# Kernel tuning notes

Hardware: AMD Instinct MI355X
Metric: run time of the kernel (lower is better)

The kernel has to match this reference:

```python
import jax, jax.numpy as jnp
import numpy as np

NUM_LEVELS = 16
LEVEL_DIM = 2
BASE_RES = 16
DESIRED_RES = 2048
HASHMAP_SIZE = 2 ** 19
MULTIRES = 6
N_POINTS = 1048576

_scale = np.exp2(np.log2(DESIRED_RES / BASE_RES) / (NUM_LEVELS - 1))
RESOLUTIONS = [int(np.ceil(BASE_RES * _scale ** l)) for l in range(NUM_LEVELS)]
PRIMES = np.array([1, 2654435761, 805459861], dtype=np.uint32)
CORNERS = np.array([[i, j, k] for i in (0, 1) for j in (0, 1) for k in (0, 1)], dtype=np.int32)  # [8,3]


def positional_embed(x):
    # NeRF embedding (include_input, log-sampled freqs 2^0..2^(M-1)) -> [N, 3 + 3*2*M] = [N,39]
    freqs = (2.0 ** jnp.arange(MULTIRES)).astype(x.dtype)        # [M]
    xb = x[:, None, :] * freqs[None, :, None]                    # [N, M, 3]
    emb = jnp.concatenate([jnp.sin(xb), jnp.cos(xb)], axis=-1)   # [N, M, 6]
    return jnp.concatenate([x, emb.reshape(x.shape[0], -1)], axis=-1)


def hash_encode(x, tables):
    # multiresolution hash-grid trilinear lookup; x in [0,1]^3 -> [N, NUM_LEVELS*LEVEL_DIM]
    corners = jnp.asarray(CORNERS)       # [8,3]
    primes = jnp.asarray(PRIMES)         # [3] uint32
    outs = []
    for l, R in enumerate(RESOLUTIONS):  # fixed 16 levels (structurally distinct)
        pos = x * (R - 1)                # [N,3]
        p0 = jnp.floor(pos)
        w = pos - p0                     # fractional part, [N,3]
        c = p0.astype(jnp.int32)[:, None, :] + corners[None]   # [N,8,3] corner coords
        c = jnp.clip(c, 0, R - 1)
        if (R ** 3) <= HASHMAP_SIZE:
            idx = c[..., 0] + R * c[..., 1] + R * R * c[..., 2]  # direct (dense) indexing
        else:
            cu = c.astype(jnp.uint32)
            h = (cu[..., 0] * primes[0]) ^ (cu[..., 1] * primes[1]) ^ (cu[..., 2] * primes[2])
            idx = (h & jnp.uint32(HASHMAP_SIZE - 1)).astype(jnp.int32)
        wc = jnp.where(corners[None].astype(bool), w[:, None, :], 1.0 - w[:, None, :])  # [N,8,3]
        wc = jnp.prod(wc, axis=-1)        # trilinear weights [N,8]
        feats = tables[l][idx]            # gather [N,8,LEVEL_DIM]
        outs.append(jnp.sum(wc[..., None] * feats, axis=1))
    return jnp.concatenate(outs, axis=-1)


def softplus100(x):
    # torch.nn.Softplus(beta=100) with default threshold=20 (linear when beta*x > 20)
    return jnp.where(x * 100.0 > 20.0, x, jax.nn.softplus(x * 100.0) / 100.0)


def setup_inputs() -> dict:
    key = jax.random.key(0)
    ks = jax.random.split(key, 8)
    D_IN = 3 + 3 * 2 * MULTIRES + NUM_LEVELS * LEVEL_DIM  # 71
    x = jax.random.uniform(ks[0], (N_POINTS, 3), dtype=jnp.float32)
    tables = jax.random.uniform(ks[1], (NUM_LEVELS, HASHMAP_SIZE, LEVEL_DIM), minval=-1e-4, maxval=1e-4, dtype=jnp.float32)
    W0 = jax.random.normal(ks[2], (64, D_IN), dtype=jnp.float32) * (np.sqrt(2.0) / np.sqrt(64.0))
    b0 = jnp.zeros((64,), jnp.float32)
    W1 = jax.random.normal(ks[3], (64, 64), dtype=jnp.float32) * (np.sqrt(2.0) / np.sqrt(64.0))
    b1 = jnp.zeros((64,), jnp.float32)
    W2 = jnp.full((17, 64), np.sqrt(np.pi) / np.sqrt(64.0), jnp.float32) + jax.random.normal(ks[4], (17, 64), dtype=jnp.float32) * 1e-4
    b2 = jnp.full((17,), -1.0, jnp.float32)  # geometric init bias
    return {"x": x, "tables": tables, "W0": W0, "b0": b0, "W1": W1, "b1": b1, "W2": W2, "b2": b2}


def reference(x, tables, W0, b0, W1, b1, W2, b2):
    # divide_factor = 1.0 -> encoding sees x directly
    feat = hash_encode(x, tables)                                   # [N,32]
    h = jnp.concatenate([positional_embed(x), feat], axis=-1)       # [N,71]
    h = softplus100(h @ W0.T + b0)                                  # [N,64]
    h = softplus100(h @ W1.T + b1)                                  # [N,64]
    return h @ W2.T + b2                                            # [N,17] = (sdf, 16 features)
```

## Files before the change

kernel.cpp:

```cpp
#include <hip/hip_runtime.h>
#include <stdint.h>

#define HMAP   (1u << 19)
#define HMASK  (HMAP - 1u)

typedef short bf16x8 __attribute__((ext_vector_type(8)));
typedef float f32x4  __attribute__((ext_vector_type(4)));
typedef float f32x2  __attribute__((ext_vector_type(2)));
typedef unsigned u32x2 __attribute__((ext_vector_type(2)));

__device__ __constant__ const int c_res[16] = {16, 23, 31, 43, 59, 81, 112, 154, 213, 295, 407, 562, 777, 1073, 1483, 2048};

__device__ __forceinline__ unsigned short f2bf(float f) {
    unsigned u = __float_as_uint(f);
    u += 0x7fffu + ((u >> 16) & 1u);
    return (unsigned short)(u >> 16);
}

__device__ __forceinline__ float softplus100(float v) {
    return fmaxf(v, 0.f) + 0.01f * __logf(1.f + __expf(-100.f * fabsf(v)));
}

__device__ __forceinline__ bf16x8 cvt8(const float* __restrict__ p) {
    f32x4 a = *(const f32x4*)p;
    f32x4 b = *(const f32x4*)(p + 4);
    bf16x8 r;
    r[0] = f2bf(a[0]); r[1] = f2bf(a[1]); r[2] = f2bf(a[2]); r[3] = f2bf(a[3]);
    r[4] = f2bf(b[0]); r[5] = f2bf(b[1]); r[6] = f2bf(b[2]); r[7] = f2bf(b[3]);
    return r;
}

__device__ __forceinline__ float2 upk(unsigned v) {
    return make_float2(__uint_as_float(v << 16), __uint_as_float(v & 0xffff0000u));
}

__device__ __forceinline__ float2 gather_level(const float* __restrict__ tab, int R,
                                               float x0, float x1, float x2) {
    const float Rm1 = (float)(R - 1);
    float px = x0 * Rm1, py = x1 * Rm1, pz = x2 * Rm1;
    float fx = floorf(px), fy = floorf(py), fz = floorf(pz);
    float wx = px - fx, wy = py - fy, wz = pz - fz;
    int ix = (int)fx, iy = (int)fy, iz = (int)fz;
    ix = max(0, min(ix, R - 1)); iy = max(0, min(iy, R - 1)); iz = max(0, min(iz, R - 1));
    int jx = min(ix + 1, R - 1), jy = min(iy + 1, R - 1), jz = min(iz + 1, R - 1);
    float ax = 1.f - wx, ay = 1.f - wy, az = 1.f - wz;
    float wyz0 = ay * az, wyz1 = wy * az, wyz2 = ay * wz, wyz3 = wy * wz;
    float2 lo[4], hi[4];
    const bool adj = (jx == ix + 1);
    if ((long long)R * R * R <= (long long)HMAP) {
        unsigned sy = (unsigned)R, sz = (unsigned)(R * R);
        unsigned bases[4] = {(unsigned)iy * sy + (unsigned)iz * sz,
                             (unsigned)jy * sy + (unsigned)iz * sz,
                             (unsigned)iy * sy + (unsigned)jz * sz,
                             (unsigned)jy * sy + (unsigned)jz * sz};
        const float2* t2 = (const float2*)tab;
        #pragma unroll
        for (int k = 0; k < 4; ++k) {
            unsigned i0 = bases[k] + (unsigned)ix;
            if (adj && !(i0 & 1u)) {
                f32x4 q = *(const f32x4*)(tab + ((size_t)i0 << 1));
                lo[k] = make_float2(q[0], q[1]);
                hi[k] = make_float2(q[2], q[3]);
            } else {
                lo[k] = t2[i0];
                hi[k] = t2[bases[k] + (unsigned)jx];
            }
        }
    } else {
        unsigned hy0 = (unsigned)iy * 2654435761u, hy1 = (unsigned)jy * 2654435761u;
        unsigned hz0 = (unsigned)iz * 805459861u,  hz1 = (unsigned)jz * 805459861u;
        unsigned ms[4] = {hy0 ^ hz0, hy1 ^ hz0, hy0 ^ hz1, hy1 ^ hz1};
        if (adj && ((ix & 1) == 0)) {
            #pragma unroll
            for (int k = 0; k < 4; ++k) {
                unsigned h = ((unsigned)ix ^ ms[k]) & HMASK;
                f32x4 q = *(const f32x4*)(tab + ((size_t)(h & ~1u) << 1));
                float2 e0 = make_float2(q[0], q[1]);
                float2 e1 = make_float2(q[2], q[3]);
                bool sw = (h & 1u) != 0;
                lo[k] = sw ? e1 : e0;
                hi[k] = sw ? e0 : e1;
            }
        } else {
            const float2* t2 = (const float2*)tab;
            #pragma unroll
            for (int k = 0; k < 4; ++k) {
                unsigned hl = ((unsigned)ix ^ ms[k]) & HMASK;
                unsigned hh = ((unsigned)jx ^ ms[k]) & HMASK;
                lo[k] = t2[hl];
                hi[k] = t2[hh];
            }
        }
    }
    float2 r = make_float2(0.f, 0.f);
    float wyz[4] = {wyz0, wyz1, wyz2, wyz3};
    #pragma unroll
    for (int k = 0; k < 4; ++k) {
        float wl = ax * wyz[k], wh = wx * wyz[k];
        r.x += wl * lo[k].x + wh * hi[k].x;
        r.y += wl * lo[k].y + wh * hi[k].y;
    }
    return r;
}

__device__ __forceinline__ void gather2(const float* __restrict__ tab, int R,
                                        float x0A, float x1A, float x2A,
                                        float x0B, float x1B, float x2B,
                                        float2& rA, float2& rB) {
    const float Rm1 = (float)(R - 1);
    float wxv[2], axv[2];
    float wyz[2][4];
    float2 lo[2][4], hi[2][4];
    int ixv[2], jxv[2];
    unsigned basev[2][4];
    const bool dense = (long long)R * R * R <= (long long)HMAP;
    #pragma unroll
    for (int t = 0; t < 2; ++t) {
        const float X0 = t ? x0B : x0A, X1 = t ? x1B : x1A, X2 = t ? x2B : x2A;
        float px = X0 * Rm1, py = X1 * Rm1, pz = X2 * Rm1;
        float fx = floorf(px), fy = floorf(py), fz = floorf(pz);
        float wx = px - fx, wy = py - fy, wz = pz - fz;
        int ix = (int)fx, iy = (int)fy, iz = (int)fz;
        ix = max(0, min(ix, R - 1)); iy = max(0, min(iy, R - 1)); iz = max(0, min(iz, R - 1));
        int jx = min(ix + 1, R - 1), jy = min(iy + 1, R - 1), jz = min(iz + 1, R - 1);
        float ax = 1.f - wx, ay = 1.f - wy, az = 1.f - wz;
        wyz[t][0] = ay * az; wyz[t][1] = wy * az; wyz[t][2] = ay * wz; wyz[t][3] = wy * wz;
        wxv[t] = wx; axv[t] = ax; ixv[t] = ix; jxv[t] = jx;
        if (dense) {
            unsigned sy = (unsigned)R, sz = (unsigned)(R * R);
            basev[t][0] = (unsigned)iy * sy + (unsigned)iz * sz;
            basev[t][1] = (unsigned)jy * sy + (unsigned)iz * sz;
            basev[t][2] = (unsigned)iy * sy + (unsigned)jz * sz;
            basev[t][3] = (unsigned)jy * sy + (unsigned)jz * sz;
        } else {
            unsigned hy0 = (unsigned)iy * 2654435761u, hy1 = (unsigned)jy * 2654435761u;
            unsigned hz0 = (unsigned)iz * 805459861u,  hz1 = (unsigned)jz * 805459861u;
            basev[t][0] = hy0 ^ hz0; basev[t][1] = hy1 ^ hz0;
            basev[t][2] = hy0 ^ hz1; basev[t][3] = hy1 ^ hz1;
        }
    }
    if (dense) {
        const float2* t2 = (const float2*)tab;
        #pragma unroll
        for (int t = 0; t < 2; ++t) {
            const bool adj = (jxv[t] == ixv[t] + 1);
            #pragma unroll
            for (int k = 0; k < 4; ++k) {
                unsigned i0 = basev[t][k] + (unsigned)ixv[t];
                if (adj && !(i0 & 1u)) {
                    f32x4 q = *(const f32x4*)(tab + ((size_t)i0 << 1));
                    lo[t][k] = make_float2(q[0], q[1]);
                    hi[t][k] = make_float2(q[2], q[3]);
                } else {
                    lo[t][k] = t2[i0];
                    hi[t][k] = t2[basev[t][k] + (unsigned)jxv[t]];
                }
            }
        }
    } else {
        const float2* t2 = (const float2*)tab;
        #pragma unroll
        for (int t = 0; t < 2; ++t) {
            const bool adj = (jxv[t] == ixv[t] + 1) && ((ixv[t] & 1) == 0);
            #pragma unroll
            for (int k = 0; k < 4; ++k) {
                if (adj) {
                    unsigned h = ((unsigned)ixv[t] ^ basev[t][k]) & HMASK;
                    f32x4 q = *(const f32x4*)(tab + ((size_t)(h & ~1u) << 1));
                    float2 e0 = make_float2(q[0], q[1]);
                    float2 e1 = make_float2(q[2], q[3]);
                    bool sw = (h & 1u) != 0;
                    lo[t][k] = sw ? e1 : e0;
                    hi[t][k] = sw ? e0 : e1;
                } else {
                    unsigned hl = ((unsigned)ixv[t] ^ basev[t][k]) & HMASK;
                    unsigned hh = ((unsigned)jxv[t] ^ basev[t][k]) & HMASK;
                    lo[t][k] = t2[hl];
                    hi[t][k] = t2[hh];
                }
            }
        }
    }
    float2 res[2];
    #pragma unroll
    for (int t = 0; t < 2; ++t) {
        float2 r = make_float2(0.f, 0.f);
        #pragma unroll
        for (int k = 0; k < 4; ++k) {
            float wl = axv[t] * wyz[t][k], wh = wxv[t] * wyz[t][k];
            r.x += wl * lo[t][k].x + wh * hi[t][k].x;
            r.y += wl * lo[t][k].y + wh * hi[t][k].y;
        }
        res[t] = r;
    }
    rA = res[0]; rB = res[1];
}

__device__ __forceinline__ void gather2h(const unsigned* __restrict__ tab, int R,
                                         float x0A, float x1A, float x2A,
                                         float x0B, float x1B, float x2B,
                                         float2& rA, float2& rB) {
    const float Rm1 = (float)(R - 1);
    float wxv[2], axv[2], wyz[2][4];
    int ixv[2], jxv[2];
    bool adjv[2];
    unsigned msv[2][4];
    #pragma unroll
    for (int t = 0; t < 2; ++t) {
        const float X0 = t ? x0B : x0A, X1 = t ? x1B : x1A, X2 = t ? x2B : x2A;
        float px = X0 * Rm1, py = X1 * Rm1, pz = X2 * Rm1;
        float fx = floorf(px), fy = floorf(py), fz = floorf(pz);
        float wx = px - fx, wy = py - fy, wz = pz - fz;
        int ix = (int)fx, iy = (int)fy, iz = (int)fz;
        ix = max(0, min(ix, R - 1)); iy = max(0, min(iy, R - 1)); iz = max(0, min(iz, R - 1));
        int jx = min(ix + 1, R - 1), jy = min(iy + 1, R - 1), jz = min(iz + 1, R - 1);
        float ax = 1.f - wx, ay = 1.f - wy, az = 1.f - wz;
        wyz[t][0] = ay * az; wyz[t][1] = wy * az; wyz[t][2] = ay * wz; wyz[t][3] = wy * wz;
        wxv[t] = wx; axv[t] = ax; ixv[t] = ix; jxv[t] = jx;
        adjv[t] = (jx == ix + 1) && ((ix & 1) == 0);
        unsigned hy0 = (unsigned)iy * 2654435761u, hy1 = (unsigned)jy * 2654435761u;
        unsigned hz0 = (unsigned)iz * 805459861u,  hz1 = (unsigned)jz * 805459861u;
        msv[t][0] = hy0 ^ hz0; msv[t][1] = hy1 ^ hz0;
        msv[t][2] = hy0 ^ hz1; msv[t][3] = hy1 ^ hz1;
    }
    float2 lo[2][4], hi[2][4];
    #pragma unroll
    for (int t = 0; t < 2; ++t) {
        #pragma unroll
        for (int k = 0; k < 4; ++k) {
            if (adjv[t]) {
                unsigned h = ((unsigned)ixv[t] ^ msv[t][k]) & HMASK;
                u32x2 q = *(const u32x2*)(tab + (h & ~1u));
                float2 e0 = upk(q[0]), e1 = upk(q[1]);
                bool sw = (h & 1u) != 0;
                lo[t][k] = sw ? e1 : e0;
                hi[t][k] = sw ? e0 : e1;
            } else {
                unsigned hl = ((unsigned)ixv[t] ^ msv[t][k]) & HMASK;
                unsigned hh = ((unsigned)jxv[t] ^ msv[t][k]) & HMASK;
                lo[t][k] = upk(tab[hl]);
                hi[t][k] = upk(tab[hh]);
            }
        }
    }
    float2 res[2];
    #pragma unroll
    for (int t = 0; t < 2; ++t) {
        float2 r = make_float2(0.f, 0.f);
        #pragma unroll
        for (int k = 0; k < 4; ++k) {
            float wl = axv[t] * wyz[t][k], wh = wxv[t] * wyz[t][k];
            r.x += wl * lo[t][k].x + wh * hi[t][k].x;
            r.y += wl * lo[t][k].y + wh * hi[t][k].y;
        }
        res[t] = r;
    }
    rA = res[0]; rB = res[1];
}

__global__ __launch_bounds__(256)
void cvt_tables(const float* __restrict__ tables, unsigned* __restrict__ tbf) {
    const size_t i = (size_t)blockIdx.x * 256 + threadIdx.x;
    const f32x2* src = (const f32x2*)(tables + (size_t)5 * 2 * HMAP);
    f32x2 f = __builtin_nontemporal_load(src + i);
    unsigned v = (unsigned)f2bf(f[0]) | ((unsigned)f2bf(f[1]) << 16);
    __builtin_nontemporal_store(v, tbf + i);
}

__global__ __launch_bounds__(256, 6)
void gather_hashed(const float* __restrict__ x, const unsigned* __restrict__ tbf,
                   unsigned* __restrict__ feat, int N) {
    const int j = blockIdx.x & 7;
    const int i = blockIdx.x >> 3;
    int level, chunk;
    if (i < 2048) {
        level = 5 + j; chunk = i;
    } else {
        const int r = i - 2048;
        if (j < 3) {
            const int share = (j == 2) ? 682 : 683;
            if (r >= share) return;
            level = 13; chunk = j * 683 + r;
        } else if (j < 6) {
            const int jj = j - 3;
            const int share = (jj == 2) ? 682 : 683;
            if (r >= share) return;
            level = 14; chunk = jj * 683 + r;
        } else {
            if (r >= 1024) return;
            level = 15; chunk = (j - 6) * 1024 + r;
        }
    }
    const size_t p0 = (size_t)chunk * 512 + 2u * threadIdx.x;
    const f32x2* xv = (const f32x2*)(x + 3 * p0);
    f32x2 u0 = __builtin_nontemporal_load(xv);
    f32x2 u1 = __builtin_nontemporal_load(xv + 1);
    f32x2 u2 = __builtin_nontemporal_load(xv + 2);
    float2 fA, fB;
    gather2h(tbf + (size_t)(level - 5) * HMAP, c_res[level],
             u0[0], u0[1], u1[0],
             u1[1], u2[0], u2[1],
             fA, fB);
    u32x2 v;
    v[0] = (unsigned)f2bf(fA.x) | ((unsigned)f2bf(fA.y) << 16);
    v[1] = (unsigned)f2bf(fB.x) | ((unsigned)f2bf(fB.y) << 16);
    __builtin_nontemporal_store(v, (u32x2*)(feat + (size_t)(level - 5) * N + p0));
}

#define NPB       128
#define TILES     8
#define PTS_BLK   (NPB * TILES)
#define SA_STRIDE 104
#define SW0_OFF   (128 * 104)
#define SMEM_SHORTS (SW0_OFF + 64 * 104)

__global__ __launch_bounds__(256, 4)
void mlp_tiled2(const float* __restrict__ x, const float* __restrict__ tables,
                const unsigned* __restrict__ feat,
                const float* __restrict__ W0, const float* __restrict__ b0,
                const float* __restrict__ W1, const float* __restrict__ b1,
                const float* __restrict__ W2, const float* __restrict__ b2,
                float* __restrict__ out, int N) {
    __shared__ unsigned short smem[SMEM_SHORTS];
    const int tid  = threadIdx.x;
    const int blk  = blockIdx.x;
    const int wave = tid >> 6, lane = tid & 63;
    const int mhalf = (wave & 1) * 64;
    const int nhalf = (wave >> 1);
    const int lrow = lane & 15, quad = lane >> 4;

    for (int i = tid; i < 64 * 104; i += 256) {
        int n = i / 104, k = i - n * 104;
        smem[SW0_OFF + i] = (k < 71) ? f2bf(W0[n * 71 + k]) : (unsigned short)0;
    }
    for (int i = tid; i < 128 * 25; i += 256) {
        int p = i / 25, k = i - p * 25;
        smem[p * SA_STRIDE + 71 + k] = 0;
    }
    bf16x8 w1f[2][2];
    #pragma unroll
    for (int ks = 0; ks < 2; ++ks)
        #pragma unroll
        for (int nt = 0; nt < 2; ++nt) {
            int n = nhalf * 32 + nt * 16 + lrow;
            w1f[ks][nt] = cvt8(W1 + n * 64 + ks * 32 + quad * 8);
        }
    bf16x8 w2f[2];
    {
        int n2 = nhalf * 16 + lrow;
        #pragma unroll
        for (int ks = 0; ks < 2; ++ks) {
            if (n2 < 17) w2f[ks] = cvt8(W2 + n2 * 64 + ks * 32 + quad * 8);
            else { bf16x8 z = {0,0,0,0,0,0,0,0}; w2f[ks] = z; }
        }
    }
    float b0v[2], b1v[2], b2v;
    #pragma unroll
    for (int nt = 0; nt < 2; ++nt) {
        b0v[nt] = b0[nhalf * 32 + nt * 16 + lrow];
        b1v[nt] = b1[nhalf * 32 + nt * 16 + lrow];
    }
    { int c2 = nhalf * 16 + lrow; b2v = (c2 < 17) ? b2[c2] : 0.f; }
    __syncthreads();

    const size_t pbase0 = (size_t)blk * PTS_BLK;
    #pragma unroll 1
    for (int t = 0; t < TILES; ++t) {
        const size_t pb = pbase0 + (size_t)t * NPB;
        {
            const int p = tid & 127;
            const size_t gp = pb + p;
            unsigned short* row = &smem[p * SA_STRIDE];
            const float x0 = __builtin_nontemporal_load(x + 3 * gp);
            const float x1 = __builtin_nontemporal_load(x + 3 * gp + 1);
            const float x2 = __builtin_nontemporal_load(x + 3 * gp + 2);
            float sa, ca, sb, cb, sc, cc;
            __sincosf(x0, &sa, &ca);
            __sincosf(x1, &sb, &cb);
            __sincosf(x2, &sc, &cc);
            if (tid < 128) {
                row[0] = f2bf(x0); row[1] = f2bf(x1); row[2] = f2bf(x2);
                #pragma unroll
                for (int m = 0; m < 6; ++m) {
                    row[3 + 6 * m + 0] = f2bf(sa);
                    row[3 + 6 * m + 1] = f2bf(sb);
                    row[3 + 6 * m + 2] = f2bf(sc);
                    float nsa = 2.f * sa * ca, nca = 1.f - 2.f * sa * sa;
                    float nsb = 2.f * sb * cb, ncb = 1.f - 2.f * sb * sb;
                    float nsc = 2.f * sc * cc, ncc = 1.f - 2.f * sc * sc;
                    sa = nsa; ca = nca; sb = nsb; cb = ncb; sc = nsc; cc = ncc;
                }
                float2 f;
                f = gather_level(tables,                         16, x0, x1, x2);
                row[39] = f2bf(f.x); row[40] = f2bf(f.y);
                f = gather_level(tables + (size_t)1 * 2 * HMAP,  23, x0, x1, x2);
                row[41] = f2bf(f.x); row[42] = f2bf(f.y);
                f = gather_level(tables + (size_t)2 * 2 * HMAP,  31, x0, x1, x2);
                row[43] = f2bf(f.x); row[44] = f2bf(f.y);
            } else {
                #pragma unroll
                for (int m = 0; m < 6; ++m) {
                    row[3 + 6 * m + 3] = f2bf(ca);
                    row[3 + 6 * m + 4] = f2bf(cb);
                    row[3 + 6 * m + 5] = f2bf(cc);
                    float nsa = 2.f * sa * ca, nca = 1.f - 2.f * sa * sa;
                    float nsb = 2.f * sb * cb, ncb = 1.f - 2.f * sb * sb;
                    float nsc = 2.f * sc * cc, ncc = 1.f - 2.f * sc * sc;
                    sa = nsa; ca = nca; sb = nsb; cb = ncb; sc = nsc; cc = ncc;
                }
                float2 f;
                f = gather_level(tables + (size_t)3 * 2 * HMAP,  43, x0, x1, x2);
                row[45] = f2bf(f.x); row[46] = f2bf(f.y);
                f = gather_level(tables + (size_t)4 * 2 * HMAP,  59, x0, x1, x2);
                row[47] = f2bf(f.x); row[48] = f2bf(f.y);
                #pragma unroll
                for (int li = 0; li < 11; ++li) {
                    unsigned v = __builtin_nontemporal_load(feat + (size_t)li * N + gp);
                    row[49 + 2 * li] = (unsigned short)(v & 0xffffu);
                    row[50 + 2 * li] = (unsigned short)(v >> 16);
                }
            }
        }
        __syncthreads();

        f32x4 acc0[4][2];
        #pragma unroll
        for (int mt = 0; mt < 4; ++mt)
            #pragma unroll
            for (int nt = 0; nt < 2; ++nt) acc0[mt][nt] = (f32x4){0.f, 0.f, 0.f, 0.f};
        #pragma unroll
        for (int ks = 0; ks < 3; ++ks) {
            bf16x8 bfr[2];
            #pragma unroll
            for (int nt = 0; nt < 2; ++nt) {
                int n = nhalf * 32 + nt * 16 + lrow;
                bfr[nt] = *(const bf16x8*)&smem[SW0_OFF + n * 104 + ks * 32 + quad * 8];
            }
            #pragma unroll
            for (int mt = 0; mt < 4; ++mt) {
                int m = mhalf + mt * 16 + lrow;
                bf16x8 afr = *(const bf16x8*)&smem[m * SA_STRIDE + ks * 32 + quad * 8];
                #pragma unroll
                for (int nt = 0; nt < 2; ++nt)
                    acc0[mt][nt] = __builtin_amdgcn_mfma_f32_16x16x32_bf16(afr, bfr[nt], acc0[mt][nt], 0, 0, 0);
            }
        }
        __syncthreads();
        #pragma unroll
        for (int mt = 0; mt < 4; ++mt)
            #pragma unroll
            for (int nt = 0; nt < 2; ++nt) {
                int colg = nhalf * 32 + nt * 16 + lrow;
                #pragma unroll
                for (int r = 0; r < 4; ++r) {
                    int rowm = mhalf + mt * 16 + quad * 4 + r;
                    smem[rowm * SA_STRIDE + colg] = f2bf(softplus100(acc0[mt][nt][r] + b0v[nt]));
                }
            }
        __syncthreads();

        f32x4 acc1[4][2];
        #pragma unroll
        for (int mt = 0; mt < 4; ++mt)
            #pragma unroll
            for (int nt = 0; nt < 2; ++nt) acc1[mt][nt] = (f32x4){0.f, 0.f, 0.f, 0.f};
        #pragma unroll
        for (int ks = 0; ks < 2; ++ks) {
            #pragma unroll
            for (int mt = 0; mt < 4; ++mt) {
                int m = mhalf + mt * 16 + lrow;
                bf16x8 afr = *(const bf16x8*)&smem[m * SA_STRIDE + ks * 32 + quad * 8];
                #pragma unroll
                for (int nt = 0; nt < 2; ++nt)
                    acc1[mt][nt] = __builtin_amdgcn_mfma_f32_16x16x32_bf16(afr, w1f[ks][nt], acc1[mt][nt], 0, 0, 0);
            }
        }
        __syncthreads();
        #pragma unroll
        for (int mt = 0; mt < 4; ++mt)
            #pragma unroll
            for (int nt = 0; nt < 2; ++nt) {
                int colg = nhalf * 32 + nt * 16 + lrow;
                #pragma unroll
                for (int r = 0; r < 4; ++r) {
                    int rowm = mhalf + mt * 16 + quad * 4 + r;
                    smem[rowm * SA_STRIDE + colg] = f2bf(softplus100(acc1[mt][nt][r] + b1v[nt]));
                }
            }
        __syncthreads();

        f32x4 acc2[4];
        #pragma unroll
        for (int mt = 0; mt < 4; ++mt) acc2[mt] = (f32x4){0.f, 0.f, 0.f, 0.f};
        #pragma unroll
        for (int ks = 0; ks < 2; ++ks) {
            #pragma unroll
            for (int mt = 0; mt < 4; ++mt) {
                int m = mhalf + mt * 16 + lrow;
                bf16x8 afr = *(const bf16x8*)&smem[m * SA_STRIDE + ks * 32 + quad * 8];
                acc2[mt] = __builtin_amdgcn_mfma_f32_16x16x32_bf16(afr, w2f[ks], acc2[mt], 0, 0, 0);
            }
        }
        {
            int colg = nhalf * 16 + lrow;
            if (colg < 17) {
                #pragma unroll
                for (int mt = 0; mt < 4; ++mt)
                    #pragma unroll
                    for (int r = 0; r < 4; ++r) {
                        int rowm = mhalf + mt * 16 + quad * 4 + r;
                        __builtin_nontemporal_store(acc2[mt][r] + b2v,
                                                    out + (pb + rowm) * 17 + colg);
                    }
            }
        }
        __syncthreads();
    }
}

__global__ __launch_bounds__(256, 6)
void gather_levels(const float* __restrict__ x, const float* __restrict__ tables,
                   unsigned* __restrict__ feat, int N, int C) {
    const int b = blockIdx.x;
    const int half = 8 * C;
    int r, level;
    if (b < half) { r = b; level = r & 7; }
    else          { r = b - half; level = 15 - (r & 7); }
    const size_t p0 = (size_t)(r >> 3) * 512 + 2u * threadIdx.x;
    const f32x2* xv = (const f32x2*)(x + 3 * p0);
    f32x2 u0 = __builtin_nontemporal_load(xv);
    f32x2 u1 = __builtin_nontemporal_load(xv + 1);
    f32x2 u2 = __builtin_nontemporal_load(xv + 2);
    float2 fA, fB;
    gather2(tables + (size_t)level * (2u * HMAP), c_res[level],
            u0[0], u0[1], u1[0],
            u1[1], u2[0], u2[1],
            fA, fB);
    u32x2 v;
    v[0] = (unsigned)f2bf(fA.x) | ((unsigned)f2bf(fA.y) << 16);
    v[1] = (unsigned)f2bf(fB.x) | ((unsigned)f2bf(fB.y) << 16);
    __builtin_nontemporal_store(v, (u32x2*)(feat + (size_t)level * N + p0));
}

__global__ __launch_bounds__(256, 4)
void mlp_tiled(const float* __restrict__ x, const unsigned* __restrict__ feat,
               const float* __restrict__ W0, const float* __restrict__ b0,
               const float* __restrict__ W1, const float* __restrict__ b1,
               const float* __restrict__ W2, const float* __restrict__ b2,
               float* __restrict__ out, int N) {
    __shared__ unsigned short smem[SMEM_SHORTS];
    const int tid  = threadIdx.x;
    const int blk  = blockIdx.x;
    const int wave = tid >> 6, lane = tid & 63;
    const int mhalf = (wave & 1) * 64;
    const int nhalf = (wave >> 1);
    const int lrow = lane & 15, quad = lane >> 4;

    for (int i = tid; i < 64 * 104; i += 256) {
        int n = i / 104, k = i - n * 104;
        smem[SW0_OFF + i] = (k < 71) ? f2bf(W0[n * 71 + k]) : (unsigned short)0;
    }
    for (int i = tid; i < 128 * 25; i += 256) {
        int p = i / 25, k = i - p * 25;
        smem[p * SA_STRIDE + 71 + k] = 0;
    }
    bf16x8 w1f[2][2];
    #pragma unroll
    for (int ks = 0; ks < 2; ++ks)
        #pragma unroll
        for (int nt = 0; nt < 2; ++nt) {
            int n = nhalf * 32 + nt * 16 + lrow;
            w1f[ks][nt] = cvt8(W1 + n * 64 + ks * 32 + quad * 8);
        }
    bf16x8 w2f[2];
    {
        int n2 = nhalf * 16 + lrow;
        #pragma unroll
        for (int ks = 0; ks < 2; ++ks) {
            if (n2 < 17) w2f[ks] = cvt8(W2 + n2 * 64 + ks * 32 + quad * 8);
            else { bf16x8 z = {0,0,0,0,0,0,0,0}; w2f[ks] = z; }
        }
    }
    float b0v[2], b1v[2], b2v;
    #pragma unroll
    for (int nt = 0; nt < 2; ++nt) {
        b0v[nt] = b0[nhalf * 32 + nt * 16 + lrow];
        b1v[nt] = b1[nhalf * 32 + nt * 16 + lrow];
    }
    { int c2 = nhalf * 16 + lrow; b2v = (c2 < 17) ? b2[c2] : 0.f; }
    __syncthreads();

    const size_t pbase0 = (size_t)blk * PTS_BLK;
    #pragma unroll 1
    for (int t = 0; t < TILES; ++t) {
        const size_t pb = pbase0 + (size_t)t * NPB;
        {
            const int p = tid & 127;
            const size_t gp = pb + p;
            unsigned short* row = &smem[p * SA_STRIDE];
            const float x0 = __builtin_nontemporal_load(x + 3 * gp);
            const float x1 = __builtin_nontemporal_load(x + 3 * gp + 1);
            const float x2 = __builtin_nontemporal_load(x + 3 * gp + 2);
            if (tid < 128) {
                row[0] = f2bf(x0); row[1] = f2bf(x1); row[2] = f2bf(x2);
                float fr = 1.f;
                #pragma unroll
                for (int m = 0; m < 6; ++m) {
                    row[3 + 6 * m + 0] = f2bf(__sinf(x0 * fr));
                    row[3 + 6 * m + 1] = f2bf(__sinf(x1 * fr));
                    row[3 + 6 * m + 2] = f2bf(__sinf(x2 * fr));
                    fr *= 2.f;
                }
            } else {
                float fr = 1.f;
                #pragma unroll
                for (int m = 0; m < 6; ++m) {
                    row[3 + 6 * m + 3] = f2bf(__cosf(x0 * fr));
                    row[3 + 6 * m + 4] = f2bf(__cosf(x1 * fr));
                    row[3 + 6 * m + 5] = f2bf(__cosf(x2 * fr));
                    fr *= 2.f;
                }
                #pragma unroll
                for (int l = 0; l < 16; ++l) {
                    unsigned v = __builtin_nontemporal_load(feat + (size_t)l * N + gp);
                    row[39 + 2 * l] = (unsigned short)(v & 0xffffu);
                    row[40 + 2 * l] = (unsigned short)(v >> 16);
                }
            }
        }
        __syncthreads();

        f32x4 acc0[4][2];
        #pragma unroll
        for (int mt = 0; mt < 4; ++mt)
            #pragma unroll
            for (int nt = 0; nt < 2; ++nt) acc0[mt][nt] = (f32x4){0.f, 0.f, 0.f, 0.f};
        #pragma unroll
        for (int ks = 0; ks < 3; ++ks) {
            bf16x8 bfr[2];
            #pragma unroll
            for (int nt = 0; nt < 2; ++nt) {
                int n = nhalf * 32 + nt * 16 + lrow;
                bfr[nt] = *(const bf16x8*)&smem[SW0_OFF + n * 104 + ks * 32 + quad * 8];
            }
            #pragma unroll
            for (int mt = 0; mt < 4; ++mt) {
                int m = mhalf + mt * 16 + lrow;
                bf16x8 afr = *(const bf16x8*)&smem[m * SA_STRIDE + ks * 32 + quad * 8];
                #pragma unroll
                for (int nt = 0; nt < 2; ++nt)
                    acc0[mt][nt] = __builtin_amdgcn_mfma_f32_16x16x32_bf16(afr, bfr[nt], acc0[mt][nt], 0, 0, 0);
            }
        }
        __syncthreads();
        #pragma unroll
        for (int mt = 0; mt < 4; ++mt)
            #pragma unroll
            for (int nt = 0; nt < 2; ++nt) {
                int colg = nhalf * 32 + nt * 16 + lrow;
                #pragma unroll
                for (int r = 0; r < 4; ++r) {
                    int rowm = mhalf + mt * 16 + quad * 4 + r;
                    smem[rowm * SA_STRIDE + colg] = f2bf(softplus100(acc0[mt][nt][r] + b0v[nt]));
                }
            }
        __syncthreads();

        f32x4 acc1[4][2];
        #pragma unroll
        for (int mt = 0; mt < 4; ++mt)
            #pragma unroll
            for (int nt = 0; nt < 2; ++nt) acc1[mt][nt] = (f32x4){0.f, 0.f, 0.f, 0.f};
        #pragma unroll
        for (int ks = 0; ks < 2; ++ks) {
            #pragma unroll
            for (int mt = 0; mt < 4; ++mt) {
                int m = mhalf + mt * 16 + lrow;
                bf16x8 afr = *(const bf16x8*)&smem[m * SA_STRIDE + ks * 32 + quad * 8];
                #pragma unroll
                for (int nt = 0; nt < 2; ++nt)
                    acc1[mt][nt] = __builtin_amdgcn_mfma_f32_16x16x32_bf16(afr, w1f[ks][nt], acc1[mt][nt], 0, 0, 0);
            }
        }
        __syncthreads();
        #pragma unroll
        for (int mt = 0; mt < 4; ++mt)
            #pragma unroll
            for (int nt = 0; nt < 2; ++nt) {
                int colg = nhalf * 32 + nt * 16 + lrow;
                #pragma unroll
                for (int r = 0; r < 4; ++r) {
                    int rowm = mhalf + mt * 16 + quad * 4 + r;
                    smem[rowm * SA_STRIDE + colg] = f2bf(softplus100(acc1[mt][nt][r] + b1v[nt]));
                }
            }
        __syncthreads();

        f32x4 acc2[4];
        #pragma unroll
        for (int mt = 0; mt < 4; ++mt) acc2[mt] = (f32x4){0.f, 0.f, 0.f, 0.f};
        #pragma unroll
        for (int ks = 0; ks < 2; ++ks) {
            #pragma unroll
            for (int mt = 0; mt < 4; ++mt) {
                int m = mhalf + mt * 16 + lrow;
                bf16x8 afr = *(const bf16x8*)&smem[m * SA_STRIDE + ks * 32 + quad * 8];
                acc2[mt] = __builtin_amdgcn_mfma_f32_16x16x32_bf16(afr, w2f[ks], acc2[mt], 0, 0, 0);
            }
        }
        {
            int colg = nhalf * 16 + lrow;
            if (colg < 17) {
                #pragma unroll
                for (int mt = 0; mt < 4; ++mt)
                    #pragma unroll
                    for (int r = 0; r < 4; ++r) {
                        int rowm = mhalf + mt * 16 + quad * 4 + r;
                        __builtin_nontemporal_store(acc2[mt][r] + b2v,
                                                    out + (pb + rowm) * 17 + colg);
                    }
            }
        }
        __syncthreads();
    }
}

__global__ __launch_bounds__(256, 3)
void gn_fused(const float* __restrict__ x, const float* __restrict__ tables,
              const float* __restrict__ W0, const float* __restrict__ b0,
              const float* __restrict__ W1, const float* __restrict__ b1,
              const float* __restrict__ W2, const float* __restrict__ b2,
              float* __restrict__ out) {
    __shared__ unsigned short smem[SMEM_SHORTS];
    const int tid = threadIdx.x;
    const int blk = blockIdx.x;
    const int wave = tid >> 6, lane = tid & 63;
    const int mhalf = (wave & 1) * 64;
    const int nhalf = (wave >> 1);
    const int lrow = lane & 15, quad = lane >> 4;
    for (int i = tid; i < 64 * 104; i += 256) {
        int n = i / 104, k = i - n * 104;
        smem[SW0_OFF + i] = (k < 71) ? f2bf(W0[n * 71 + k]) : (unsigned short)0;
    }
    for (int i = tid; i < 128 * 25; i += 256) {
        int p = i / 25, k = i - p * 25;
        smem[p * SA_STRIDE + 71 + k] = 0;
    }
    bf16x8 w1f[2][2];
    #pragma unroll
    for (int ks = 0; ks < 2; ++ks)
        #pragma unroll
        for (int nt = 0; nt < 2; ++nt) {
            int n = nhalf * 32 + nt * 16 + lrow;
            w1f[ks][nt] = cvt8(W1 + n * 64 + ks * 32 + quad * 8);
        }
    bf16x8 w2f[2];
    {
        int n2 = nhalf * 16 + lrow;
        #pragma unroll
        for (int ks = 0; ks < 2; ++ks) {
            if (n2 < 17) w2f[ks] = cvt8(W2 + n2 * 64 + ks * 32 + quad * 8);
            else { bf16x8 z = {0,0,0,0,0,0,0,0}; w2f[ks] = z; }
        }
    }
    float b0v[2], b1v[2], b2v;
    #pragma unroll
    for (int nt = 0; nt < 2; ++nt) {
        b0v[nt] = b0[nhalf * 32 + nt * 16 + lrow];
        b1v[nt] = b1[nhalf * 32 + nt * 16 + lrow];
    }
    { int c2 = nhalf * 16 + lrow; b2v = (c2 < 17) ? b2[c2] : 0.f; }
    {
        const int p = tid & 127;
        const size_t gp = (size_t)blk * NPB + p;
        const float x0 = x[3 * gp], x1 = x[3 * gp + 1], x2 = x[3 * gp + 2];
        unsigned short* row = &smem[p * SA_STRIDE];
        if (tid < 128) {
            row[0] = f2bf(x0); row[1] = f2bf(x1); row[2] = f2bf(x2);
            float fr = 1.f;
            #pragma unroll
            for (int m = 0; m < 6; ++m) {
                row[3 + 6 * m + 0] = f2bf(__sinf(x0 * fr));
                row[3 + 6 * m + 1] = f2bf(__sinf(x1 * fr));
                row[3 + 6 * m + 2] = f2bf(__sinf(x2 * fr));
                fr *= 2.f;
            }
            #pragma unroll
            for (int li = 0; li < 8; ++li) {
                const int l = 2 * li;
                float2 f = gather_level(tables + (size_t)l * (2u * HMAP), c_res[l], x0, x1, x2);
                row[39 + 2 * l] = f2bf(f.x);
                row[40 + 2 * l] = f2bf(f.y);
            }
        } else {
            float fr = 1.f;
            #pragma unroll
            for (int m = 0; m < 6; ++m) {
                row[3 + 6 * m + 3] = f2bf(__cosf(x0 * fr));
                row[3 + 6 * m + 4] = f2bf(__cosf(x1 * fr));
                row[3 + 6 * m + 5] = f2bf(__cosf(x2 * fr));
                fr *= 2.f;
            }
            #pragma unroll
            for (int li = 0; li < 8; ++li) {
                const int l = 2 * li + 1;
                float2 f = gather_level(tables + (size_t)l * (2u * HMAP), c_res[l], x0, x1, x2);
                row[39 + 2 * l] = f2bf(f.x);
                row[40 + 2 * l] = f2bf(f.y);
            }
        }
    }
    __syncthreads();
    f32x4 acc0[4][2];
    #pragma unroll
    for (int mt = 0; mt < 4; ++mt)
        #pragma unroll
        for (int nt = 0; nt < 2; ++nt) acc0[mt][nt] = (f32x4){0.f, 0.f, 0.f, 0.f};
    #pragma unroll
    for (int ks = 0; ks < 3; ++ks) {
        bf16x8 bfr[2];
        #pragma unroll
        for (int nt = 0; nt < 2; ++nt) {
            int n = nhalf * 32 + nt * 16 + lrow;
            bfr[nt] = *(const bf16x8*)&smem[SW0_OFF + n * 104 + ks * 32 + quad * 8];
        }
        #pragma unroll
        for (int mt = 0; mt < 4; ++mt) {
            int m = mhalf + mt * 16 + lrow;
            bf16x8 afr = *(const bf16x8*)&smem[m * SA_STRIDE + ks * 32 + quad * 8];
            #pragma unroll
            for (int nt = 0; nt < 2; ++nt)
                acc0[mt][nt] = __builtin_amdgcn_mfma_f32_16x16x32_bf16(afr, bfr[nt], acc0[mt][nt], 0, 0, 0);
        }
    }
    __syncthreads();
    #pragma unroll
    for (int mt = 0; mt < 4; ++mt)
        #pragma unroll
        for (int nt = 0; nt < 2; ++nt) {
            int colg = nhalf * 32 + nt * 16 + lrow;
            #pragma unroll
            for (int r = 0; r < 4; ++r) {
                int rowm = mhalf + mt * 16 + quad * 4 + r;
                smem[rowm * SA_STRIDE + colg] = f2bf(softplus100(acc0[mt][nt][r] + b0v[nt]));
            }
        }
    __syncthreads();
    f32x4 acc1[4][2];
    #pragma unroll
    for (int mt = 0; mt < 4; ++mt)
        #pragma unroll
        for (int nt = 0; nt < 2; ++nt) acc1[mt][nt] = (f32x4){0.f, 0.f, 0.f, 0.f};
    #pragma unroll
    for (int ks = 0; ks < 2; ++ks) {
        #pragma unroll
        for (int mt = 0; mt < 4; ++mt) {
            int m = mhalf + mt * 16 + lrow;
            bf16x8 afr = *(const bf16x8*)&smem[m * SA_STRIDE + ks * 32 + quad * 8];
            #pragma unroll
            for (int nt = 0; nt < 2; ++nt)
                acc1[mt][nt] = __builtin_amdgcn_mfma_f32_16x16x32_bf16(afr, w1f[ks][nt], acc1[mt][nt], 0, 0, 0);
        }
    }
    __syncthreads();
    #pragma unroll
    for (int mt = 0; mt < 4; ++mt)
        #pragma unroll
        for (int nt = 0; nt < 2; ++nt) {
            int colg = nhalf * 32 + nt * 16 + lrow;
            #pragma unroll
            for (int r = 0; r < 4; ++r) {
                int rowm = mhalf + mt * 16 + quad * 4 + r;
                smem[rowm * SA_STRIDE + colg] = f2bf(softplus100(acc1[mt][nt][r] + b1v[nt]));
            }
        }
    __syncthreads();
    f32x4 acc2[4];
    #pragma unroll
    for (int mt = 0; mt < 4; ++mt) acc2[mt] = (f32x4){0.f, 0.f, 0.f, 0.f};
    #pragma unroll
    for (int ks = 0; ks < 2; ++ks) {
        #pragma unroll
        for (int mt = 0; mt < 4; ++mt) {
            int m = mhalf + mt * 16 + lrow;
            bf16x8 afr = *(const bf16x8*)&smem[m * SA_STRIDE + ks * 32 + quad * 8];
            acc2[mt] = __builtin_amdgcn_mfma_f32_16x16x32_bf16(afr, w2f[ks], acc2[mt], 0, 0, 0);
        }
    }
    {
        int colg = nhalf * 16 + lrow;
        if (colg < 17) {
            #pragma unroll
            for (int mt = 0; mt < 4; ++mt)
                #pragma unroll
                for (int r = 0; r < 4; ++r) {
                    int rowm = mhalf + mt * 16 + quad * 4 + r;
                    out[((size_t)blk * NPB + rowm) * 17 + colg] = acc2[mt][r] + b2v;
                }
        }
    }
}

extern "C" void kernel_launch(void* const* d_in, const int* in_sizes, int n_in,
                              void* d_out, int out_size, void* d_ws, size_t ws_size,
                              hipStream_t stream) {
    const float* x      = (const float*)d_in[0];
    const float* tables = (const float*)d_in[1];
    const float* W0     = (const float*)d_in[2];
    const float* b0     = (const float*)d_in[3];
    const float* W1     = (const float*)d_in[4];
    const float* b1     = (const float*)d_in[5];
    const float* W2     = (const float*)d_in[6];
    const float* b2     = (const float*)d_in[7];
    float* out = (float*)d_out;
    const int n = in_sizes[0] / 3;
    const size_t featA_b = (size_t)11 * n * 4;
    const size_t tbf_b   = (size_t)11 * HMAP * 4;
    const size_t wsB     = (size_t)16 * n * 4;
    if (n == (1 << 20) && ws_size >= featA_b + tbf_b) {
        unsigned* feat = (unsigned*)d_ws;
        unsigned* tbf  = (unsigned*)((char*)d_ws + featA_b);
        cvt_tables<<<dim3(11 * HMAP / 256), dim3(256), 0, stream>>>(tables, tbf);
        gather_hashed<<<dim3(8 * 3072), dim3(256), 0, stream>>>(x, tbf, feat, n);
        mlp_tiled2<<<dim3(n / PTS_BLK), dim3(256), 0, stream>>>(x, tables, feat, W0, b0, W1, b1, W2, b2, out, n);
    } else if (ws_size >= wsB) {
        unsigned* feat = (unsigned*)d_ws;
        const int C = n / 512;
        gather_levels<<<dim3(16 * C), dim3(256), 0, stream>>>(x, tables, feat, n, C);
        mlp_tiled<<<dim3(n / PTS_BLK), dim3(256), 0, stream>>>(x, feat, W0, b0, W1, b1, W2, b2, out, n);
    } else {
        gn_fused<<<dim3(n / NPB), dim3(256), 0, stream>>>(x, tables, W0, b0, W1, b1, W2, b2, out);
    }
}
```

Baseline: 549.4 us.

## Reorder MLP input layout for packed bf16 stores and raise gather occupancy

Permutes the first-layer input columns so the embedding and features land on 32-bit aligned pairs. This lets the staging code write packed bf16 words using v_cvt_pk_bf16_f32 instead of many scalar 16-bit LDS stores, and the W0 shared-memory copy is reordered to match. Hidden-layer activations are also converted two at a time with the packed instruction. The gather kernel's launch bound is raised from 6 to 8 blocks per CU, which trades register budget for occupancy, and other kernels get a separate smem offset macro.

```diff
diff --git a/kernel.cpp b/kernel.cpp
--- a/kernel.cpp
+++ b/kernel.cpp
@@ -15,6 +15,12 @@
     unsigned u = __float_as_uint(f);
     u += 0x7fffu + ((u >> 16) & 1u);
     return (unsigned short)(u >> 16);
+}
+
+__device__ __forceinline__ unsigned pk_bf16(float a, float b) {
+    unsigned r;
+    asm("v_cvt_pk_bf16_f32 %0, %1, %2" : "=v"(r) : "v"(a), "v"(b));
+    return r;
 }
 
 __device__ __forceinline__ float softplus100(float v) {
@@ -267,7 +273,7 @@
     __builtin_nontemporal_store(v, tbf + i);
 }
 
-__global__ __launch_bounds__(256, 6)
+__global__ __launch_bounds__(256, 8)
 void gather_hashed(const float* __restrict__ x, const unsigned* __restrict__ tbf,
                    unsigned* __restrict__ feat, int N) {
     const int j = blockIdx.x & 7;
@@ -330,12 +336,17 @@
     const int lrow = lane & 15, quad = lane >> 4;
 
     for (int i = tid; i < 64 * 104; i += 256) {
-        int n = i / 104, k = i - n * 104;
-        smem[SW0_OFF + i] = (k < 71) ? f2bf(W0[n * 71 + k]) : (unsigned short)0;
-    }
-    for (int i = tid; i < 128 * 25; i += 256) {
-        int p = i / 25, k = i - p * 25;
-        smem[p * SA_STRIDE + 71 + k] = 0;
+        int n = i / 104, c = i - n * 104;
+        float w = 0.f;
+        if (c < 3)                 w = W0[n * 71 + c];
+        else if (c >= 4 && c < 22) { int q = c - 4;  w = W0[n * 71 + 3 + 6 * (q / 3) + (q % 3)]; }
+        else if (c >= 22 && c < 40){ int q = c - 22; w = W0[n * 71 + 6 + 6 * (q / 3) + (q % 3)]; }
+        else if (c >= 40 && c < 72) w = W0[n * 71 + 39 + (c - 40)];
+        smem[SW0_OFF + i] = f2bf(w);
+    }
+    for (int i = tid; i < 128 * 24; i += 256) {
+        int p = i / 24, k = i - p * 24;
+        smem[p * SA_STRIDE + 72 + k] = 0;
     }
     bf16x8 w1f[2][2];
     #pragma unroll
@@ -371,6 +382,7 @@
             const int p = tid & 127;
             const size_t gp = pb + p;
             unsigned short* row = &smem[p * SA_STRIDE];
+            unsigned* row32 = (unsigned*)row;
             const float x0 = __builtin_nontemporal_load(x + 3 * gp);
             const float x1 = __builtin_nontemporal_load(x + 3 * gp + 1);
             const float x2 = __builtin_nontemporal_load(x + 3 * gp + 2);
@@ -379,46 +391,48 @@
             __sincosf(x1, &sb, &cb);
             __sincosf(x2, &sc, &cc);
             if (tid < 128) {
-                row[0] = f2bf(x0); row[1] = f2bf(x1); row[2] = f2bf(x2);
+                row32[0] = pk_bf16(x0, x1);
+                row32[1] = pk_bf16(x2, 0.f);
+                float sv[18];
                 #pragma unroll
                 for (int m = 0; m < 6; ++m) {
-                    row[3 + 6 * m + 0] = f2bf(sa);
-                    row[3 + 6 * m + 1] = f2bf(sb);
-                    row[3 + 6 * m + 2] = f2bf(sc);
+                    sv[3 * m] = sa; sv[3 * m + 1] = sb; sv[3 * m + 2] = sc;
                     float nsa = 2.f * sa * ca, nca = 1.f - 2.f * sa * sa;
                     float nsb = 2.f * sb * cb, ncb = 1.f - 2.f * sb * sb;
                     float nsc = 2.f * sc * cc, ncc = 1.f - 2.f * sc * sc;
                     sa = nsa; ca = nca; sb = nsb; cb = ncb; sc = nsc; cc = ncc;
                 }
+                #pragma unroll
+                for (int j = 0; j < 9; ++j)
+                    row32[2 + j] = pk_bf16(sv[2 * j], sv[2 * j + 1]);
                 float2 f;
                 f = gather_level(tables,                         16, x0, x1, x2);
-                row[39] = f2bf(f.x); row[40] = f2bf(f.y);
+                row32[20] = pk_bf16(f.x, f.y);
                 f = gather_level(tables + (size_t)1 * 2 * HMAP,  23, x0, x1, x2);
-                row[41] = f2bf(f.x); row[42] = f2bf(f.y);
+                row32[21] = pk_bf16(f.x, f.y);
                 f = gather_level(tables + (size_t)2 * 2 * HMAP,  31, x0, x1, x2);
-                row[43] = f2bf(f.x); row[44] = f2bf(f.y);
+                row32[22] = pk_bf16(f.x, f.y);
             } else {
+                float cv[18];
                 #pragma unroll
                 for (int m = 0; m < 6; ++m) {
-                    row[3 + 6 * m + 3] = f2bf(ca);
-                    row[3 + 6 * m + 4] = f2bf(cb);
-                    row[3 + 6 * m + 5] = f2bf(cc);
+                    cv[3 * m] = ca; cv[3 * m + 1] = cb; cv[3 * m + 2] = cc;
                     float nsa = 2.f * sa * ca, nca = 1.f - 2.f * sa * sa;
                     float nsb = 2.f * sb * cb, ncb = 1.f - 2.f * sb * sb;
                     float nsc = 2.f * sc * cc, ncc = 1.f - 2.f * sc * sc;
                     sa = nsa; ca = nca; sb = nsb; cb = ncb; sc = nsc; cc = ncc;
                 }
+                #pragma unroll
+                for (int j = 0; j < 9; ++j)
+                    row32[11 + j] = pk_bf16(cv[2 * j], cv[2 * j + 1]);
                 float2 f;
                 f = gather_level(tables + (size_t)3 * 2 * HMAP,  43, x0, x1, x2);
-                row[45] = f2bf(f.x); row[46] = f2bf(f.y);
+                row32[23] = pk_bf16(f.x, f.y);
                 f = gather_level(tables + (size_t)4 * 2 * HMAP,  59, x0, x1, x2);
-                row[47] = f2bf(f.x); row[48] = f2bf(f.y);
-                #pragma unroll
-                for (int li = 0; li < 11; ++li) {
-                    unsigned v = __builtin_nontemporal_load(feat + (size_t)li * N + gp);
-                    row[49 + 2 * li] = (unsigned short)(v & 0xffffu);
-                    row[50 + 2 * li] = (unsigned short)(v >> 16);
-                }
+                row32[24] = pk_bf16(f.x, f.y);
+                #pragma unroll
+                for (int li = 0; li < 11; ++li)
+                    row32[25 + li] = __builtin_nontemporal_load(feat + (size_t)li * N + gp);
             }
         }
         __syncthreads();
@@ -449,13 +463,14 @@
         #pragma unroll
         for (int mt = 0; mt < 4; ++mt)
             #pragma unroll
-            for (int nt = 0; nt < 2; ++nt) {
-                int colg = nhalf * 32 + nt * 16 + lrow;
-                #pragma unroll
-                for (int r = 0; r < 4; ++r) {
-                    int rowm = mhalf + mt * 16 + quad * 4 + r;
-                    smem[rowm * SA_STRIDE + colg] = f2bf(softplus100(acc0[mt][nt][r] + b0v[nt]));
-                }
+            for (int r = 0; r < 4; ++r) {
+                int rowm = mhalf + mt * 16 + quad * 4 + r;
+                float v0 = softplus100(acc0[mt][0][r] + b0v[0]);
+                float v1 = softplus100(acc0[mt][1][r] + b0v[1]);
+                unsigned pk = pk_bf16(v0, v1);
+                int c0 = nhalf * 32 + lrow;
+                smem[rowm * SA_STRIDE + c0]      = (unsigned short)pk;
+                smem[rowm * SA_STRIDE + c0 + 16] = (unsigned short)(pk >> 16);
             }
         __syncthreads();
 
@@ -479,13 +494,14 @@
         #pragma unroll
         for (int mt = 0; mt < 4; ++mt)
             #pragma unroll
-            for (int nt = 0; nt < 2; ++nt) {
-                int colg = nhalf * 32 + nt * 16 + lrow;
-                #pragma unroll
-                for (int r = 0; r < 4; ++r) {
-                    int rowm = mhalf + mt * 16 + quad * 4 + r;
-                    smem[rowm * SA_STRIDE + colg] = f2bf(softplus100(acc1[mt][nt][r] + b1v[nt]));
-                }
+            for (int r = 0; r < 4; ++r) {
+                int rowm = mhalf + mt * 16 + quad * 4 + r;
+                float v0 = softplus100(acc1[mt][0][r] + b1v[0]);
+                float v1 = softplus100(acc1[mt][1][r] + b1v[1]);
+                unsigned pk = pk_bf16(v0, v1);
+                int c0 = nhalf * 32 + lrow;
+                smem[rowm * SA_STRIDE + c0]      = (unsigned short)pk;
+                smem[rowm * SA_STRIDE + c0 + 16] = (unsigned short)(pk >> 16);
             }
         __syncthreads();
 
@@ -517,6 +533,9 @@
         __syncthreads();
     }
 }
+
+#define SW0B_OFF   (128 * 104)
+#define SMEMB_SHORTS (SW0B_OFF + 64 * 104)
 
 __global__ __launch_bounds__(256, 6)
 void gather_levels(const float* __restrict__ x, const float* __restrict__ tables,
@@ -548,7 +567,7 @@
                const float* __restrict__ W1, const float* __restrict__ b1,
                const float* __restrict__ W2, const float* __restrict__ b2,
                float* __restrict__ out, int N) {
-    __shared__ unsigned short smem[SMEM_SHORTS];
+    __shared__ unsigned short smem[SMEMB_SHORTS];
     const int tid  = threadIdx.x;
     const int blk  = blockIdx.x;
     const int wave = tid >> 6, lane = tid & 63;
@@ -558,7 +577,7 @@
 
     for (int i = tid; i < 64 * 104; i += 256) {
         int n = i / 104, k = i - n * 104;
-        smem[SW0_OFF + i] = (k < 71) ? f2bf(W0[n * 71 + k]) : (unsigned short)0;
+        smem[SW0B_OFF + i] = (k < 71) ? f2bf(W0[n * 71 + k]) : (unsigned short)0;
     }
     for (int i = tid; i < 128 * 25; i += 256) {
         int p = i / 25, k = i - p * 25;
@@ -641,7 +660,7 @@
             #pragma unroll
             for (int nt = 0; nt < 2; ++nt) {
                 int n = nhalf * 32 + nt * 16 + lrow;
-                bfr[nt] = *(const bf16x8*)&smem[SW0_OFF + n * 104 + ks * 32 + quad * 8];
+                bfr[nt] = *(const bf16x8*)&smem[SW0B_OFF + n * 104 + ks * 32 + quad * 8];
             }
             #pragma unroll
             for (int mt = 0; mt < 4; ++mt) {
@@ -731,7 +750,7 @@
               const float* __restrict__ W1, const float* __restrict__ b1,
               const float* __restrict__ W2, const float* __restrict__ b2,
               float* __restrict__ out) {
-    __shared__ unsigned short smem[SMEM_SHORTS];
+    __shared__ unsigned short smem[SMEMB_SHORTS];
     const int tid = threadIdx.x;
     const int blk = blockIdx.x;
     const int wave = tid >> 6, lane = tid & 63;
@@ -740,7 +759,7 @@
     const int lrow = lane & 15, quad = lane >> 4;
     for (int i = tid; i < 64 * 104; i += 256) {
         int n = i / 104, k = i - n * 104;
-        smem[SW0_OFF + i] = (k < 71) ? f2bf(W0[n * 71 + k]) : (unsigned short)0;
+        smem[SW0B_OFF + i] = (k < 71) ? f2bf(W0[n * 71 + k]) : (unsigned short)0;
     }
     for (int i = tid; i < 128 * 25; i += 256) {
         int p = i / 25, k = i - p * 25;
@@ -822,7 +841,7 @@
         #pragma unroll
         for (int nt = 0; nt < 2; ++nt) {
             int n = nhalf * 32 + nt * 16 + lrow;
-            bfr[nt] = *(const bf16x8*)&smem[SW0_OFF + n * 104 + ks * 32 + quad * 8];
+            bfr[nt] = *(const bf16x8*)&smem[SW0B_OFF + n * 104 + ks * 32 + quad * 8];
         }
         #pragma unroll
         for (int mt = 0; mt < 4; ++mt) {
```

After: 553.2 us. No clear change (+0.7%).
